# Optimization experiments

Hardware: AMD Instinct MI355X
Metric: run time of the kernel (lower is better)

Reference implementation:

```python
import jax, jax.numpy as jnp
import numpy as np

B, S, H, D = 2, 2048, 16, 64


def setup_inputs() -> dict:
    key = jax.random.key(0)
    kq, kk, kv, km = jax.random.split(key, 4)
    q = jax.random.normal(kq, (B, S, H, D), dtype=jnp.float32)
    k = jax.random.normal(kk, (B, S, H, D), dtype=jnp.float32)
    v = jax.random.normal(kv, (B, S, H, D), dtype=jnp.float32)
    key_padding_mask = jax.random.randint(km, (B, S), 0, 2).astype(bool)
    return {"q": q, "k": k, "v": v, "key_padding_mask": key_padding_mask}


def reference(q, k, v, key_padding_mask):
    # [B,S,H,D] -> [B,H,S,D]; fp32 upcast (inputs already fp32)
    qt = jnp.transpose(q, (0, 2, 1, 3)).astype(jnp.float32)
    kt = jnp.transpose(k, (0, 2, 1, 3)).astype(jnp.float32)
    vt = jnp.transpose(v, (0, 2, 1, 3)).astype(jnp.float32)
    scale = D ** (-0.5)
    # [B,H,Sq,Sk]
    scores = jnp.einsum("bhqd,bhkd->bhqk", qt, kt) * scale
    # masked_fill where key_padding_mask is True -> -inf
    mask = key_padding_mask[:, None, None, :]  # [B,1,1,Sk]
    scores = jnp.where(mask, -jnp.inf, scores)
    attn = jax.nn.softmax(scores, axis=-1)
    out = jnp.einsum("bhqk,bhkd->bhqd", attn, vt).astype(q.dtype)
    # back to [B,S,H,D]
    return jnp.transpose(out, (0, 2, 1, 3))
```

## Files before the change

kernel.cpp:

```cpp
#include <hip/hip_runtime.h>
#include <hip/hip_bf16.h>

#define BB 2
#define SS 2048
#define HH 16
#define DD 64
#define BR 256
#define NQT2 (SS / BR)
#define BC 64
#define NT (SS / BC)
#define TILE_E (BC * DD)
#define TILE_B (TILE_E * 2)
#define LOG2E 1.44269504f
#define OSZ (BB * SS * HH * DD)
#define VSTR 516

typedef __attribute__((ext_vector_type(8))) short short8;
typedef __attribute__((ext_vector_type(4))) float f32x4;
typedef __attribute__((ext_vector_type(16))) float f32x16;
typedef __attribute__((ext_vector_type(4))) unsigned int uint32x4;
typedef __attribute__((ext_vector_type(4))) unsigned short ushort4_t;

static __device__ __forceinline__ unsigned short f2bf(float f) {
    unsigned int u = __float_as_uint(f);
    unsigned int r = u + 0x7FFFu + ((u >> 16) & 1u);
    return (unsigned short)(r >> 16);
}
static __device__ __forceinline__ unsigned int cvtpk(float lo, float hi) {
    unsigned int r;
    asm("v_cvt_pk_bf16_f32 %0, %1, %2" : "=v"(r) : "v"(lo), "v"(hi));
    return r;
}
static __device__ __forceinline__ void pl32swap(unsigned int &a, unsigned int &b) {
#if __has_builtin(__builtin_amdgcn_permlane32_swap)
    const auto r = __builtin_amdgcn_permlane32_swap((int)a, (int)b, false, false);
    a = (unsigned int)r[0];
    b = (unsigned int)r[1];
#else
    asm("v_permlane32_swap_b32 %0, %1" : "+v"(a), "+v"(b));
#endif
}
static __device__ __forceinline__ float fexp2(float x) {
#if __has_builtin(__builtin_amdgcn_exp2f)
    return __builtin_amdgcn_exp2f(x);
#else
    return exp2f(x);
#endif
}
static __device__ __forceinline__ void gl_lds16(const void* g, void* l) {
    __builtin_amdgcn_global_load_lds(
        (const __attribute__((address_space(1))) void*)g,
        (__attribute__((address_space(3))) void*)l, 16, 0, 0);
}

__global__ __launch_bounds__(256, 2)
void prep_kernel(const float* __restrict__ K, const float* __restrict__ V,
                 const int* __restrict__ M,
                 unsigned short* __restrict__ Kb, unsigned short* __restrict__ Vt,
                 int* __restrict__ mcnt)
{
    __shared__ unsigned short VL[64 * VSTR];

    const int blk = blockIdx.x;
    const int hg  = blk & 1;
    const int t   = (blk >> 1) & 31;
    const int b   = blk >> 6;
    const int tid = threadIdx.x;

    const int* mrow = M + (size_t)b * SS + t * BC;
    const size_t rowf = (size_t)HH * DD;
    const float* kbase = K + ((size_t)b * SS + t * BC) * rowf + hg * 512;
    const float* vbase = V + ((size_t)b * SS + t * BC) * rowf + hg * 512;

    const int w  = (tid * 4) & 511;
    const int r0 = tid >> 7;
    const int hl = w >> 6;
    const int d  = w & 63;
    const int h  = hg * 8 + hl;
    const int c  = d >> 3;
    const int j  = d & 7;
    const size_t ktile = ((size_t)(b * 16 + h) * NT + t) * TILE_E;

    #pragma unroll 4
    for (int i = 0; i < 32; ++i) {
        const int r = i * 2 + r0;
        const float sel = mrow[r] ? 0.0f : 1.0f;
        const float4 fk = *(const float4*)(kbase + (size_t)r * rowf + w);
        uint2 ko;
        ko.x = cvtpk(fk.x * sel, fk.y * sel);
        ko.y = cvtpk(fk.z * sel, fk.w * sel);
        *(uint2*)(Kb + ktile + r * 64 + ((c ^ (r & 7)) * 8) + j) = ko;
        const float4 fv = *(const float4*)(vbase + (size_t)r * rowf + w);
        uint2 vo;
        vo.x = cvtpk(fv.x * sel, fv.y * sel);
        vo.y = cvtpk(fv.z * sel, fv.w * sel);
        *(uint2*)(VL + r * VSTR + w) = vo;
    }
    __syncthreads();

    #pragma unroll 4
    for (int it = 0; it < 16; ++it) {
        const int U  = it * 256 + tid;
        const int g  = U & 7;
        const int dd = (U >> 3) & 63;
        const int h2l = U >> 9;
        const int col = h2l * 64 + dd;
        unsigned int wv[4];
        #pragma unroll
        for (int jp = 0; jp < 4; ++jp) {
            const unsigned int lo = VL[(g * 8 + 2 * jp + 0) * VSTR + col];
            const unsigned int hi = VL[(g * 8 + 2 * jp + 1) * VSTR + col];
            wv[jp] = lo | (hi << 16);
        }
        uint32x4 uu;
        uu[0] = wv[0]; uu[1] = wv[1]; uu[2] = wv[2]; uu[3] = wv[3];
        const size_t vtile = ((size_t)(b * 16 + hg * 8 + h2l) * NT + t) * TILE_E;
        *(uint32x4*)(Vt + vtile + dd * 64 + ((g ^ (dd & 7)) * 8)) = uu;
    }

    if (hg == 0 && tid < 64) {
        const unsigned long long bal = __ballot(mrow[tid] != 0);
        if (tid == 0) mcnt[b * NT + t] = (int)__popcll(bal);
    }
}

__global__ __launch_bounds__(256, 2)
void fa3_kernel(const float* __restrict__ Q,
                const unsigned short* __restrict__ Kb,
                const unsigned short* __restrict__ Vt,
                const int* __restrict__ mcnt,
                float* __restrict__ Op)
{
    __shared__ __align__(16) unsigned short Ks[2][2 * TILE_E];
    __shared__ __align__(16) unsigned short Vs[2][2 * TILE_E];

    const int nwg  = BB * HH * NQT2;
    const int cpx  = nwg >> 3;
    const int blk  = (blockIdx.x & 7) * cpx + (blockIdx.x >> 3);

    const int qt  = blk & (NQT2 - 1);
    const int bh  = (blk >> 3) & 31;
    const int b   = bh >> 4;
    const int h   = bh & 15;

    const int tid  = threadIdx.x;
    const int wave = tid >> 6;
    const int lane = tid & 63;
    const int ln   = lane & 31;
    const int l5   = lane >> 5;

    const float qscale = 0.125f * LOG2E;
    const int qrowA = qt * BR + wave * 64 + ln;
    const float* qpA = Q + (((size_t)b * SS + qrowA) * HH + h) * DD;
    const float* qpB = qpA + (size_t)32 * HH * DD;
    short8 qfA[4], qfB[4];
    #pragma unroll
    for (int t = 0; t < 4; ++t) {
        const int d0 = t * 16 + l5 * 8;
        {
            const float4 f0 = *(const float4*)(qpA + d0);
            const float4 f1 = *(const float4*)(qpA + d0 + 4);
            uint32x4 u;
            u[0] = cvtpk(f0.x * qscale, f0.y * qscale);
            u[1] = cvtpk(f0.z * qscale, f0.w * qscale);
            u[2] = cvtpk(f1.x * qscale, f1.y * qscale);
            u[3] = cvtpk(f1.z * qscale, f1.w * qscale);
            qfA[t] = __builtin_bit_cast(short8, u);
        }
        {
            const float4 f0 = *(const float4*)(qpB + d0);
            const float4 f1 = *(const float4*)(qpB + d0 + 4);
            uint32x4 u;
            u[0] = cvtpk(f0.x * qscale, f0.y * qscale);
            u[1] = cvtpk(f0.z * qscale, f0.w * qscale);
            u[2] = cvtpk(f1.x * qscale, f1.y * qscale);
            u[3] = cvtpk(f1.z * qscale, f1.w * qscale);
            qfB[t] = __builtin_bit_cast(short8, u);
        }
    }

    int corr = 0;
    for (int i = 0; i < NT; ++i) corr += mcnt[b * NT + i];

    f32x16 acc0A, acc1A, acc0B, acc1B;
    #pragma unroll
    for (int i = 0; i < 16; ++i) {
        acc0A[i] = 0.f; acc1A[i] = 0.f; acc0B[i] = 0.f; acc1B[i] = 0.f;
    }
    f32x4 lsumA4 = {0.f, 0.f, 0.f, 0.f};
    f32x4 lsumB4 = {0.f, 0.f, 0.f, 0.f};

    const unsigned short* kb_bh = Kb + (size_t)bh * NT * TILE_E;
    const unsigned short* vt_bh = Vt + (size_t)bh * NT * TILE_E;
    const int we = wave * 1024;
    const int wb = wave * 2048;

    {
        const unsigned short* kbt = kb_bh;
        const unsigned short* vtt = vt_bh;
        #pragma unroll
        for (int s = 0; s < 2; ++s) {
            gl_lds16(kbt + s * TILE_E + we + lane * 8,       (char*)Ks[0] + s * TILE_B + wb);
            gl_lds16(kbt + s * TILE_E + we + 512 + lane * 8, (char*)Ks[0] + s * TILE_B + wb + 1024);
            gl_lds16(vtt + s * TILE_E + we + lane * 8,       (char*)Vs[0] + s * TILE_B + wb);
            gl_lds16(vtt + s * TILE_E + we + 512 + lane * 8, (char*)Vs[0] + s * TILE_B + wb + 1024);
        }
    }
    __syncthreads();

    const int pswz = (ln & 7);
    const int npair = NT >> 1;

    auto softmax_pack = [&](const f32x16& s0, const f32x16& s1,
                            f32x4& lsum4, short8* pf) {
        unsigned int pk[2][8];
        #pragma unroll
        for (int hh = 0; hh < 2; ++hh) {
            #pragma unroll
            for (int g = 0; g < 4; ++g) {
                const float p0 = fexp2(hh ? s1[g * 4 + 0] : s0[g * 4 + 0]);
                const float p1 = fexp2(hh ? s1[g * 4 + 1] : s0[g * 4 + 1]);
                const float p2 = fexp2(hh ? s1[g * 4 + 2] : s0[g * 4 + 2]);
                const float p3 = fexp2(hh ? s1[g * 4 + 3] : s0[g * 4 + 3]);
                lsum4 += (f32x4){p0, p1, p2, p3};
                pk[hh][g * 2 + 0] = cvtpk(p0, p1);
                pk[hh][g * 2 + 1] = cvtpk(p2, p3);
            }
        }
        #pragma unroll
        for (int hh = 0; hh < 2; ++hh) {
            pl32swap(pk[hh][0], pk[hh][2]);
            pl32swap(pk[hh][1], pk[hh][3]);
            pl32swap(pk[hh][4], pk[hh][6]);
            pl32swap(pk[hh][5], pk[hh][7]);
        }
        #pragma unroll
        for (int t = 0; t < 4; ++t) {
            const int hh = t >> 1;
            const int s4 = (t & 1) * 4;
            uint32x4 u;
            u[0] = pk[hh][s4 + 0];
            u[1] = pk[hh][s4 + 1];
            u[2] = pk[hh][s4 + 2];
            u[3] = pk[hh][s4 + 3];
            pf[t] = __builtin_bit_cast(short8, u);
        }
    };

    for (int ii = 0; ii < npair; ++ii) {
        const int cur = ii & 1;
        const int nxt = cur ^ 1;
        const int kn = 2 * ((ii + 1 < npair) ? ii + 1 : ii);
        const unsigned short* kbt = kb_bh + (size_t)kn * TILE_E;
        const unsigned short* vtt = vt_bh + (size_t)kn * TILE_E;
        #pragma unroll
        for (int s = 0; s < 2; ++s) {
            gl_lds16(kbt + s * TILE_E + we + lane * 8,       (char*)Ks[nxt] + s * TILE_B + wb);
            gl_lds16(kbt + s * TILE_E + we + 512 + lane * 8, (char*)Ks[nxt] + s * TILE_B + wb + 1024);
            gl_lds16(vtt + s * TILE_E + we + lane * 8,       (char*)Vs[nxt] + s * TILE_B + wb);
            gl_lds16(vtt + s * TILE_E + we + 512 + lane * 8, (char*)Vs[nxt] + s * TILE_B + wb + 1024);
        }

        #pragma unroll
        for (int sub = 0; sub < 2; ++sub) {
            const unsigned short* Kt = Ks[cur] + sub * TILE_E;
            const unsigned short* Vtl = Vs[cur] + sub * TILE_E;

            f32x16 sA0, sA1, sB0, sB1;
            #pragma unroll
            for (int i = 0; i < 16; ++i) {
                sA0[i] = 0.f; sA1[i] = 0.f; sB0[i] = 0.f; sB1[i] = 0.f;
            }
            #pragma unroll
            for (int t = 0; t < 4; ++t) {
                const int p = (2 * t + l5) ^ pswz;
                const short8 kf0 = *(const short8*)(Kt + ln * 64 + p * 8);
                const short8 kf1 = *(const short8*)(Kt + (32 + ln) * 64 + p * 8);
                sA0 = __builtin_amdgcn_mfma_f32_32x32x16_bf16(kf0, qfA[t], sA0, 0, 0, 0);
                sA1 = __builtin_amdgcn_mfma_f32_32x32x16_bf16(kf1, qfA[t], sA1, 0, 0, 0);
                sB0 = __builtin_amdgcn_mfma_f32_32x32x16_bf16(kf0, qfB[t], sB0, 0, 0, 0);
                sB1 = __builtin_amdgcn_mfma_f32_32x32x16_bf16(kf1, qfB[t], sB1, 0, 0, 0);
            }

            short8 pfA[4], pfB[4];
            softmax_pack(sA0, sA1, lsumA4, pfA);
            softmax_pack(sB0, sB1, lsumB4, pfB);

            #pragma unroll
            for (int t = 0; t < 4; ++t) {
                const int p = (2 * t + l5) ^ pswz;
                const short8 vf0 = *(const short8*)(Vtl + ln * 64 + p * 8);
                const short8 vf1 = *(const short8*)(Vtl + (32 + ln) * 64 + p * 8);
                acc0A = __builtin_amdgcn_mfma_f32_32x32x16_bf16(vf0, pfA[t], acc0A, 0, 0, 0);
                acc1A = __builtin_amdgcn_mfma_f32_32x32x16_bf16(vf1, pfA[t], acc1A, 0, 0, 0);
                acc0B = __builtin_amdgcn_mfma_f32_32x32x16_bf16(vf0, pfB[t], acc0B, 0, 0, 0);
                acc1B = __builtin_amdgcn_mfma_f32_32x32x16_bf16(vf1, pfB[t], acc1B, 0, 0, 0);
            }
        }

        __syncthreads();
    }

    const float lsA = (lsumA4[0] + lsumA4[1]) + (lsumA4[2] + lsumA4[3]);
    const float lsB = (lsumB4[0] + lsumB4[1]) + (lsumB4[2] + lsumB4[3]);
    const float lA = lsA + __shfl_xor(lsA, 32) - (float)corr;
    const float lB = lsB + __shfl_xor(lsB, 32) - (float)corr;
    {
        const float inv = 1.0f / lA;
        float* op = Op + (((size_t)b * SS + qrowA) * HH + h) * DD;
        #pragma unroll
        for (int dh = 0; dh < 2; ++dh) {
            #pragma unroll
            for (int g = 0; g < 4; ++g) {
                const int d0 = dh * 32 + 8 * g + 4 * l5;
                float4 o;
                o.x = (dh ? acc1A[g * 4 + 0] : acc0A[g * 4 + 0]) * inv;
                o.y = (dh ? acc1A[g * 4 + 1] : acc0A[g * 4 + 1]) * inv;
                o.z = (dh ? acc1A[g * 4 + 2] : acc0A[g * 4 + 2]) * inv;
                o.w = (dh ? acc1A[g * 4 + 3] : acc0A[g * 4 + 3]) * inv;
                *(float4*)(op + d0) = o;
            }
        }
    }
    {
        const float inv = 1.0f / lB;
        float* op = Op + (((size_t)b * SS + qrowA + 32) * HH + h) * DD;
        #pragma unroll
        for (int dh = 0; dh < 2; ++dh) {
            #pragma unroll
            for (int g = 0; g < 4; ++g) {
                const int d0 = dh * 32 + 8 * g + 4 * l5;
                float4 o;
                o.x = (dh ? acc1B[g * 4 + 0] : acc0B[g * 4 + 0]) * inv;
                o.y = (dh ? acc1B[g * 4 + 1] : acc0B[g * 4 + 1]) * inv;
                o.z = (dh ? acc1B[g * 4 + 2] : acc0B[g * 4 + 2]) * inv;
                o.w = (dh ? acc1B[g * 4 + 3] : acc0B[g * 4 + 3]) * inv;
                *(float4*)(op + d0) = o;
            }
        }
    }
}

#define KP 72
#define FBR 64
__global__ __launch_bounds__(256, 2)
void fa_fallback(const float* __restrict__ Q, const float* __restrict__ K,
                 const float* __restrict__ V, const int* __restrict__ M,
                 float* __restrict__ O)
{
    __shared__ unsigned short KsF[BC][KP];
    __shared__ unsigned short VsF[DD][KP];
    __shared__ unsigned short PsF[4][16][KP];
    __shared__ float mb[BC];

    const int blk = blockIdx.x;
    const int qt = blk % (SS / FBR);
    const int bh = blk / (SS / FBR);
    const int b = bh / HH;
    const int h = bh % HH;
    const int tid = threadIdx.x;
    const int wave = tid >> 6;
    const int lane = tid & 63;
    const int lq = lane & 15;
    const int quad = lane >> 4;

    const int qrow = qt * FBR + wave * 16 + lq;
    const float* qp = Q + (((size_t)b * SS + qrow) * HH + h) * DD;
    short8 qf[2];
    #pragma unroll
    for (int c = 0; c < 2; ++c) {
        const float4 f0 = *(const float4*)(qp + c * 32 + quad * 8);
        const float4 f1 = *(const float4*)(qp + c * 32 + quad * 8 + 4);
        short8 t;
        t[0] = (short)f2bf(f0.x * 0.125f); t[1] = (short)f2bf(f0.y * 0.125f);
        t[2] = (short)f2bf(f0.z * 0.125f); t[3] = (short)f2bf(f0.w * 0.125f);
        t[4] = (short)f2bf(f1.x * 0.125f); t[5] = (short)f2bf(f1.y * 0.125f);
        t[6] = (short)f2bf(f1.z * 0.125f); t[7] = (short)f2bf(f1.w * 0.125f);
        qf[c] = t;
    }
    f32x4 acc[4];
    #pragma unroll
    for (int dt = 0; dt < 4; ++dt) acc[dt] = (f32x4){0.f, 0.f, 0.f, 0.f};
    float m_i[4] = {-1e30f, -1e30f, -1e30f, -1e30f};
    float l_i[4] = {0.f, 0.f, 0.f, 0.f};

    const int sr = tid >> 2;
    const int sc = tid & 3;
    const size_t rowstride = (size_t)HH * DD;
    const float* kbase = K + (((size_t)b * SS) * HH + h) * DD;
    const float* vbase = V + (((size_t)b * SS) * HH + h) * DD;

    for (int kt = 0; kt < NT; ++kt) {
        const int k0 = kt * BC;
        __syncthreads();
        {
            const float* kp = kbase + (size_t)(k0 + sr) * rowstride + sc * 16;
            #pragma unroll
            for (int i = 0; i < 4; ++i) {
                const float4 f = *(const float4*)(kp + i * 4);
                ushort4_t u;
                u[0] = f2bf(f.x); u[1] = f2bf(f.y); u[2] = f2bf(f.z); u[3] = f2bf(f.w);
                *(ushort4_t*)&KsF[sr][sc * 16 + i * 4] = u;
            }
            const float* vp = vbase + (size_t)(k0 + sr) * rowstride + sc * 16;
            #pragma unroll
            for (int i = 0; i < 4; ++i) {
                const float4 f = *(const float4*)(vp + i * 4);
                const int d = sc * 16 + i * 4;
                VsF[d + 0][sr] = f2bf(f.x); VsF[d + 1][sr] = f2bf(f.y);
                VsF[d + 2][sr] = f2bf(f.z); VsF[d + 3][sr] = f2bf(f.w);
            }
            if (tid < BC) mb[tid] = M[(size_t)b * SS + k0 + tid] ? -1e30f : 0.0f;
        }
        __syncthreads();
        f32x4 s[4];
        #pragma unroll
        for (int ct = 0; ct < 4; ++ct) {
            f32x4 z = (f32x4){0.f, 0.f, 0.f, 0.f};
            const unsigned short* kr = &KsF[ct * 16 + lq][quad * 8];
            const short8 kf0 = *(const short8*)kr;
            const short8 kf1 = *(const short8*)(kr + 32);
            z = __builtin_amdgcn_mfma_f32_16x16x32_bf16(qf[0], kf0, z, 0, 0, 0);
            z = __builtin_amdgcn_mfma_f32_16x16x32_bf16(qf[1], kf1, z, 0, 0, 0);
            s[ct] = z;
        }
        #pragma unroll
        for (int ct = 0; ct < 4; ++ct) {
            const float mbias = mb[ct * 16 + lq];
            s[ct][0] += mbias; s[ct][1] += mbias; s[ct][2] += mbias; s[ct][3] += mbias;
        }
        #pragma unroll
        for (int r = 0; r < 4; ++r) {
            float mx = fmaxf(fmaxf(s[0][r], s[1][r]), fmaxf(s[2][r], s[3][r]));
            mx = fmaxf(mx, __shfl_xor(mx, 1));
            mx = fmaxf(mx, __shfl_xor(mx, 2));
            mx = fmaxf(mx, __shfl_xor(mx, 4));
            mx = fmaxf(mx, __shfl_xor(mx, 8));
            const float m_new = fmaxf(m_i[r], mx);
            const float alpha = __expf(m_i[r] - m_new);
            m_i[r] = m_new;
            float rs = 0.f;
            #pragma unroll
            for (int ct = 0; ct < 4; ++ct) {
                const float p = __expf(s[ct][r] - m_new);
                rs += p;
                PsF[wave][quad * 4 + r][ct * 16 + lq] = f2bf(p);
            }
            rs += __shfl_xor(rs, 1); rs += __shfl_xor(rs, 2);
            rs += __shfl_xor(rs, 4); rs += __shfl_xor(rs, 8);
            l_i[r] = l_i[r] * alpha + rs;
            #pragma unroll
            for (int dt = 0; dt < 4; ++dt) acc[dt][r] *= alpha;
        }
        const unsigned short* pr = &PsF[wave][lq][quad * 8];
        const short8 pf0 = *(const short8*)pr;
        const short8 pf1 = *(const short8*)(pr + 32);
        #pragma unroll
        for (int dt = 0; dt < 4; ++dt) {
            const unsigned short* vr = &VsF[dt * 16 + lq][quad * 8];
            const short8 vf0 = *(const short8*)vr;
            const short8 vf1 = *(const short8*)(vr + 32);
            acc[dt] = __builtin_amdgcn_mfma_f32_16x16x32_bf16(pf0, vf0, acc[dt], 0, 0, 0);
            acc[dt] = __builtin_amdgcn_mfma_f32_16x16x32_bf16(pf1, vf1, acc[dt], 0, 0, 0);
        }
    }
    #pragma unroll
    for (int r = 0; r < 4; ++r) {
        const float inv = 1.0f / l_i[r];
        const int row = qt * FBR + wave * 16 + quad * 4 + r;
        float* op = O + (((size_t)b * SS + row) * HH + h) * DD;
        #pragma unroll
        for (int dt = 0; dt < 4; ++dt)
            op[dt * 16 + lq] = acc[dt][r] * inv;
    }
}

extern "C" void kernel_launch(void* const* d_in, const int* in_sizes, int n_in,
                              void* d_out, int out_size, void* d_ws, size_t ws_size,
                              hipStream_t stream) {
    const float* q = (const float*)d_in[0];
    const float* k = (const float*)d_in[1];
    const float* v = (const float*)d_in[2];
    const int*   m = (const int*)d_in[3];
    float* out = (float*)d_out;

    const int nprep = BB * NT * 2;
    const size_t kb_bytes = (size_t)BB * HH * NT * TILE_E * 2;
    const size_t mc_bytes = (size_t)BB * NT * 4;
    const size_t need_single = 2 * kb_bytes + mc_bytes;

    if (ws_size >= need_single) {
        unsigned short* Kb = (unsigned short*)d_ws;
        unsigned short* Vt = (unsigned short*)((char*)d_ws + kb_bytes);
        int* mcnt = (int*)((char*)d_ws + 2 * kb_bytes);
        prep_kernel<<<nprep, 256, 0, stream>>>(k, v, m, Kb, Vt, mcnt);
        fa3_kernel<<<BB * HH * NQT2, 256, 0, stream>>>(q, Kb, Vt, mcnt, out);
    } else {
        fa_fallback<<<BB * HH * (SS / FBR), 256, 0, stream>>>(q, k, v, m, out);
    }
}
```

Baseline: 139.2 us.

## Halve query tile to 128 rows, one 32-row MFMA group per wave

Each workgroup now covers 128 query rows instead of 256, with each wave handling 32 rows instead of two 32-row groups. This doubles the workgroup count (512 vs 256) to fill the GPU's compute units better and lowers register pressure from the accumulators. The cost is that each loaded K/V tile in LDS is reused by half as many query rows, doubling global K/V traffic.

```diff
diff --git a/kernel.cpp b/kernel.cpp
--- a/kernel.cpp
+++ b/kernel.cpp
@@ -5,8 +5,8 @@
 #define SS 2048
 #define HH 16
 #define DD 64
-#define BR 256
-#define NQT2 (SS / BR)
+#define BR 128
+#define NQT (SS / BR)
 #define BC 64
 #define NT (SS / BC)
 #define TILE_E (BC * DD)
@@ -134,12 +134,12 @@
     __shared__ __align__(16) unsigned short Ks[2][2 * TILE_E];
     __shared__ __align__(16) unsigned short Vs[2][2 * TILE_E];
 
-    const int nwg  = BB * HH * NQT2;
+    const int nwg  = BB * HH * NQT;
     const int cpx  = nwg >> 3;
     const int blk  = (blockIdx.x & 7) * cpx + (blockIdx.x >> 3);
 
-    const int qt  = blk & (NQT2 - 1);
-    const int bh  = (blk >> 3) & 31;
+    const int qt  = blk & (NQT - 1);
+    const int bh  = (blk >> 4) & 31;
     const int b   = bh >> 4;
     const int h   = bh & 15;
 
@@ -150,45 +150,29 @@
     const int l5   = lane >> 5;
 
     const float qscale = 0.125f * LOG2E;
-    const int qrowA = qt * BR + wave * 64 + ln;
-    const float* qpA = Q + (((size_t)b * SS + qrowA) * HH + h) * DD;
-    const float* qpB = qpA + (size_t)32 * HH * DD;
-    short8 qfA[4], qfB[4];
+    const int qrow = qt * BR + wave * 32 + ln;
+    const float* qp = Q + (((size_t)b * SS + qrow) * HH + h) * DD;
+    short8 qf[4];
     #pragma unroll
     for (int t = 0; t < 4; ++t) {
         const int d0 = t * 16 + l5 * 8;
-        {
-            const float4 f0 = *(const float4*)(qpA + d0);
-            const float4 f1 = *(const float4*)(qpA + d0 + 4);
-            uint32x4 u;
-            u[0] = cvtpk(f0.x * qscale, f0.y * qscale);
-            u[1] = cvtpk(f0.z * qscale, f0.w * qscale);
-            u[2] = cvtpk(f1.x * qscale, f1.y * qscale);
-            u[3] = cvtpk(f1.z * qscale, f1.w * qscale);
-            qfA[t] = __builtin_bit_cast(short8, u);
-        }
-        {
-            const float4 f0 = *(const float4*)(qpB + d0);
-            const float4 f1 = *(const float4*)(qpB + d0 + 4);
-            uint32x4 u;
-            u[0] = cvtpk(f0.x * qscale, f0.y * qscale);
-            u[1] = cvtpk(f0.z * qscale, f0.w * qscale);
-            u[2] = cvtpk(f1.x * qscale, f1.y * qscale);
-            u[3] = cvtpk(f1.z * qscale, f1.w * qscale);
-            qfB[t] = __builtin_bit_cast(short8, u);
-        }
+        const float4 f0 = *(const float4*)(qp + d0);
+        const float4 f1 = *(const float4*)(qp + d0 + 4);
+        uint32x4 u;
+        u[0] = cvtpk(f0.x * qscale, f0.y * qscale);
+        u[1] = cvtpk(f0.z * qscale, f0.w * qscale);
+        u[2] = cvtpk(f1.x * qscale, f1.y * qscale);
+        u[3] = cvtpk(f1.z * qscale, f1.w * qscale);
+        qf[t] = __builtin_bit_cast(short8, u);
     }
 
     int corr = 0;
     for (int i = 0; i < NT; ++i) corr += mcnt[b * NT + i];
 
-    f32x16 acc0A, acc1A, acc0B, acc1B;
-    #pragma unroll
-    for (int i = 0; i < 16; ++i) {
-        acc0A[i] = 0.f; acc1A[i] = 0.f; acc0B[i] = 0.f; acc1B[i] = 0.f;
-    }
-    f32x4 lsumA4 = {0.f, 0.f, 0.f, 0.f};
-    f32x4 lsumB4 = {0.f, 0.f, 0.f, 0.f};
+    f32x16 acc0, acc1;
+    #pragma unroll
+    for (int i = 0; i < 16; ++i) { acc0[i] = 0.f; acc1[i] = 0.f; }
+    f32x4 lsum4 = {0.f, 0.f, 0.f, 0.f};
 
     const unsigned short* kb_bh = Kb + (size_t)bh * NT * TILE_E;
     const unsigned short* vt_bh = Vt + (size_t)bh * NT * TILE_E;
@@ -210,42 +194,6 @@
 
     const int pswz = (ln & 7);
     const int npair = NT >> 1;
-
-    auto softmax_pack = [&](const f32x16& s0, const f32x16& s1,
-                            f32x4& lsum4, short8* pf) {
-        unsigned int pk[2][8];
-        #pragma unroll
-        for (int hh = 0; hh < 2; ++hh) {
-            #pragma unroll
-            for (int g = 0; g < 4; ++g) {
-                const float p0 = fexp2(hh ? s1[g * 4 + 0] : s0[g * 4 + 0]);
-                const float p1 = fexp2(hh ? s1[g * 4 + 1] : s0[g * 4 + 1]);
-                const float p2 = fexp2(hh ? s1[g * 4 + 2] : s0[g * 4 + 2]);
-                const float p3 = fexp2(hh ? s1[g * 4 + 3] : s0[g * 4 + 3]);
-                lsum4 += (f32x4){p0, p1, p2, p3};
-                pk[hh][g * 2 + 0] = cvtpk(p0, p1);
-                pk[hh][g * 2 + 1] = cvtpk(p2, p3);
-            }
-        }
-        #pragma unroll
-        for (int hh = 0; hh < 2; ++hh) {
-            pl32swap(pk[hh][0], pk[hh][2]);
-            pl32swap(pk[hh][1], pk[hh][3]);
-            pl32swap(pk[hh][4], pk[hh][6]);
-            pl32swap(pk[hh][5], pk[hh][7]);
-        }
-        #pragma unroll
-        for (int t = 0; t < 4; ++t) {
-            const int hh = t >> 1;
-            const int s4 = (t & 1) * 4;
-            uint32x4 u;
-            u[0] = pk[hh][s4 + 0];
-            u[1] = pk[hh][s4 + 1];
-            u[2] = pk[hh][s4 + 2];
-            u[3] = pk[hh][s4 + 3];
-            pf[t] = __builtin_bit_cast(short8, u);
-        }
-    };
 
     for (int ii = 0; ii < npair; ++ii) {
         const int cur = ii & 1;
@@ -266,77 +214,80 @@
             const unsigned short* Kt = Ks[cur] + sub * TILE_E;
             const unsigned short* Vtl = Vs[cur] + sub * TILE_E;
 
-            f32x16 sA0, sA1, sB0, sB1;
-            #pragma unroll
-            for (int i = 0; i < 16; ++i) {
-                sA0[i] = 0.f; sA1[i] = 0.f; sB0[i] = 0.f; sB1[i] = 0.f;
-            }
+            f32x16 s0, s1;
+            #pragma unroll
+            for (int i = 0; i < 16; ++i) { s0[i] = 0.f; s1[i] = 0.f; }
             #pragma unroll
             for (int t = 0; t < 4; ++t) {
                 const int p = (2 * t + l5) ^ pswz;
                 const short8 kf0 = *(const short8*)(Kt + ln * 64 + p * 8);
                 const short8 kf1 = *(const short8*)(Kt + (32 + ln) * 64 + p * 8);
-                sA0 = __builtin_amdgcn_mfma_f32_32x32x16_bf16(kf0, qfA[t], sA0, 0, 0, 0);
-                sA1 = __builtin_amdgcn_mfma_f32_32x32x16_bf16(kf1, qfA[t], sA1, 0, 0, 0);
-                sB0 = __builtin_amdgcn_mfma_f32_32x32x16_bf16(kf0, qfB[t], sB0, 0, 0, 0);
-                sB1 = __builtin_amdgcn_mfma_f32_32x32x16_bf16(kf1, qfB[t], sB1, 0, 0, 0);
-            }
-
-            short8 pfA[4], pfB[4];
-            softmax_pack(sA0, sA1, lsumA4, pfA);
-            softmax_pack(sB0, sB1, lsumB4, pfB);
+                s0 = __builtin_amdgcn_mfma_f32_32x32x16_bf16(kf0, qf[t], s0, 0, 0, 0);
+                s1 = __builtin_amdgcn_mfma_f32_32x32x16_bf16(kf1, qf[t], s1, 0, 0, 0);
+            }
+
+            unsigned int pk[2][8];
+            #pragma unroll
+            for (int hh = 0; hh < 2; ++hh) {
+                #pragma unroll
+                for (int g = 0; g < 4; ++g) {
+                    const float p0 = fexp2(hh ? s1[g * 4 + 0] : s0[g * 4 + 0]);
+                    const float p1 = fexp2(hh ? s1[g * 4 + 1] : s0[g * 4 + 1]);
+                    const float p2 = fexp2(hh ? s1[g * 4 + 2] : s0[g * 4 + 2]);
+                    const float p3 = fexp2(hh ? s1[g * 4 + 3] : s0[g * 4 + 3]);
+                    lsum4 += (f32x4){p0, p1, p2, p3};
+                    pk[hh][g * 2 + 0] = cvtpk(p0, p1);
+                    pk[hh][g * 2 + 1] = cvtpk(p2, p3);
+                }
+            }
+            #pragma unroll
+            for (int hh = 0; hh < 2; ++hh) {
+                pl32swap(pk[hh][0], pk[hh][2]);
+                pl32swap(pk[hh][1], pk[hh][3]);
+                pl32swap(pk[hh][4], pk[hh][6]);
+                pl32swap(pk[hh][5], pk[hh][7]);
+            }
+            short8 pf[4];
+            #pragma unroll
+            for (int t = 0; t < 4; ++t) {
+                const int hh = t >> 1;
+                const int s4 = (t & 1) * 4;
+                uint32x4 u;
+                u[0] = pk[hh][s4 + 0];
+                u[1] = pk[hh][s4 + 1];
+                u[2] = pk[hh][s4 + 2];
+                u[3] = pk[hh][s4 + 3];
+                pf[t] = __builtin_bit_cast(short8, u);
+            }
 
             #pragma unroll
             for (int t = 0; t < 4; ++t) {
                 const int p = (2 * t + l5) ^ pswz;
                 const short8 vf0 = *(const short8*)(Vtl + ln * 64 + p * 8);
                 const short8 vf1 = *(const short8*)(Vtl + (32 + ln) * 64 + p * 8);
-                acc0A = __builtin_amdgcn_mfma_f32_32x32x16_bf16(vf0, pfA[t], acc0A, 0, 0, 0);
-                acc1A = __builtin_amdgcn_mfma_f32_32x32x16_bf16(vf1, pfA[t], acc1A, 0, 0, 0);
-                acc0B = __builtin_amdgcn_mfma_f32_32x32x16_bf16(vf0, pfB[t], acc0B, 0, 0, 0);
-                acc1B = __builtin_amdgcn_mfma_f32_32x32x16_bf16(vf1, pfB[t], acc1B, 0, 0, 0);
+                acc0 = __builtin_amdgcn_mfma_f32_32x32x16_bf16(vf0, pf[t], acc0, 0, 0, 0);
+                acc1 = __builtin_amdgcn_mfma_f32_32x32x16_bf16(vf1, pf[t], acc1, 0, 0, 0);
             }
         }
 
         __syncthreads();
     }
 
-    const float lsA = (lsumA4[0] + lsumA4[1]) + (lsumA4[2] + lsumA4[3]);
-    const float lsB = (lsumB4[0] + lsumB4[1]) + (lsumB4[2] + lsumB4[3]);
-    const float lA = lsA + __shfl_xor(lsA, 32) - (float)corr;
-    const float lB = lsB + __shfl_xor(lsB, 32) - (float)corr;
-    {
-        const float inv = 1.0f / lA;
-        float* op = Op + (((size_t)b * SS + qrowA) * HH + h) * DD;
-        #pragma unroll
-        for (int dh = 0; dh < 2; ++dh) {
-            #pragma unroll
-            for (int g = 0; g < 4; ++g) {
-                const int d0 = dh * 32 + 8 * g + 4 * l5;
-                float4 o;
-                o.x = (dh ? acc1A[g * 4 + 0] : acc0A[g * 4 + 0]) * inv;
-                o.y = (dh ? acc1A[g * 4 + 1] : acc0A[g * 4 + 1]) * inv;
-                o.z = (dh ? acc1A[g * 4 + 2] : acc0A[g * 4 + 2]) * inv;
-                o.w = (dh ? acc1A[g * 4 + 3] : acc0A[g * 4 + 3]) * inv;
-                *(float4*)(op + d0) = o;
-            }
-        }
-    }
-    {
-        const float inv = 1.0f / lB;
-        float* op = Op + (((size_t)b * SS + qrowA + 32) * HH + h) * DD;
-        #pragma unroll
-        for (int dh = 0; dh < 2; ++dh) {
-            #pragma unroll
-            for (int g = 0; g < 4; ++g) {
-                const int d0 = dh * 32 + 8 * g + 4 * l5;
-                float4 o;
-                o.x = (dh ? acc1B[g * 4 + 0] : acc0B[g * 4 + 0]) * inv;
-                o.y = (dh ? acc1B[g * 4 + 1] : acc0B[g * 4 + 1]) * inv;
-                o.z = (dh ? acc1B[g * 4 + 2] : acc0B[g * 4 + 2]) * inv;
-                o.w = (dh ? acc1B[g * 4 + 3] : acc0B[g * 4 + 3]) * inv;
-                *(float4*)(op + d0) = o;
-            }
+    const float lsum = (lsum4[0] + lsum4[1]) + (lsum4[2] + lsum4[3]);
+    const float l = lsum + __shfl_xor(lsum, 32) - (float)corr;
+    const float inv = 1.0f / l;
+    float* op = Op + (((size_t)b * SS + qrow) * HH + h) * DD;
+    #pragma unroll
+    for (int dh = 0; dh < 2; ++dh) {
+        #pragma unroll
+        for (int g = 0; g < 4; ++g) {
+            const int d0 = dh * 32 + 8 * g + 4 * l5;
+            float4 o;
+            o.x = (dh ? acc1[g * 4 + 0] : acc0[g * 4 + 0]) * inv;
+            o.y = (dh ? acc1[g * 4 + 1] : acc0[g * 4 + 1]) * inv;
+            o.z = (dh ? acc1[g * 4 + 2] : acc0[g * 4 + 2]) * inv;
+            o.w = (dh ? acc1[g * 4 + 3] : acc0[g * 4 + 3]) * inv;
+            *(float4*)(op + d0) = o;
         }
     }
 }
@@ -494,7 +445,7 @@
         unsigned short* Vt = (unsigned short*)((char*)d_ws + kb_bytes);
         int* mcnt = (int*)((char*)d_ws + 2 * kb_bytes);
         prep_kernel<<<nprep, 256, 0, stream>>>(k, v, m, Kb, Vt, mcnt);
-        fa3_kernel<<<BB * HH * NQT2, 256, 0, stream>>>(q, Kb, Vt, mcnt, out);
+        fa3_kernel<<<BB * HH * NQT, 256, 0, stream>>>(q, Kb, Vt, mcnt, out);
     } else {
         fa_fallback<<<BB * HH * (SS / FBR), 256, 0, stream>>>(q, k, v, m, out);
     }
```

Measured after the change: 136.5 us, median of 2. Within noise of the previous version (-1.9%).
